# Kernel tuning notes

Measured on AMD Instinct MI355X. Metric: run time of the kernel, lower is better.

## Reference

```python
import jax, jax.numpy as jnp
import numpy as np

EPS = 1e-5

def rmsnorm(x, w):
    var = jnp.mean(x * x, axis=-1, keepdims=True)
    return x * jax.lax.rsqrt(var + EPS) * w

def apply_rope(x, cos, sin):
    # x: [B, S, H, D], cos/sin: [S, D//2]; llama-style complex rotation over pairs
    B, S, H, D = x.shape
    xr = x.reshape(B, S, H, D // 2, 2)
    x0, x1 = xr[..., 0], xr[..., 1]
    c = cos[None, :, None, :]
    s = sin[None, :, None, :]
    o0 = x0 * c - x1 * s
    o1 = x0 * s + x1 * c
    return jnp.stack([o0, o1], axis=-1).reshape(B, S, H, D)

def setup_inputs() -> dict:
    key = jax.random.key(0)
    ks = jax.random.split(key, 8)
    B, S, dim = 2, 2048, 2048
    H, nope, rope = 16, 128, 64
    q_lr, kv_lr = 1536, 512
    hd = nope + rope
    x = jax.random.normal(ks[0], (B, S, dim), jnp.float32)
    wd_q = jax.random.normal(ks[1], (dim, q_lr), jnp.float32) * (dim ** -0.5)
    wu_q = jax.random.normal(ks[2], (q_lr, H * hd), jnp.float32) * (q_lr ** -0.5)
    q_norm_w = jnp.ones((q_lr,), jnp.float32)
    wd_kv = jax.random.normal(ks[3], (dim, kv_lr + rope), jnp.float32) * (dim ** -0.5)
    wu_kv = jax.random.normal(ks[4], (kv_lr, H * 2 * nope), jnp.float32) * (kv_lr ** -0.5)
    kv_norm_w = jnp.ones((kv_lr,), jnp.float32)
    wo = jax.random.normal(ks[5], (H * nope, dim), jnp.float32) * ((H * nope) ** -0.5)
    pos = jnp.arange(S, dtype=jnp.float32)
    inv_freq = 1.0 / (10000.0 ** (jnp.arange(0, rope, 2, dtype=jnp.float32) / rope))
    ang = pos[:, None] * inv_freq[None, :]  # [S, rope//2]
    return {"x": x, "wd_q": wd_q, "wu_q": wu_q, "q_norm_w": q_norm_w,
            "wd_kv": wd_kv, "wu_kv": wu_kv, "kv_norm_w": kv_norm_w, "wo": wo,
            "cos": jnp.cos(ang), "sin": jnp.sin(ang), "start_pos": 0}

def reference(x, wd_q, wu_q, q_norm_w, wd_kv, wu_kv, kv_norm_w, wo, cos, sin, start_pos):
    B, S, dim = x.shape
    H, nope, rope = 16, 128, 64
    kv_lr = 512
    hd = nope + rope
    # low-rank Q projection + RMSNorm
    cq = x @ wd_q
    xq = rmsnorm(cq, q_norm_w) @ wu_q
    xq = xq.reshape(B, S, H, hd)
    xq_nope, xq_rope = xq[..., :nope], xq[..., nope:]
    # low-rank KV projection
    kvd = x @ wd_kv
    ckv, xk_rope = kvd[..., :kv_lr], kvd[..., kv_lr:]
    xk_rope = xk_rope.reshape(B, S, 1, rope)
    kvu = (rmsnorm(ckv, kv_norm_w) @ wu_kv).reshape(B, S, H, 2 * nope)
    xk_nope, xv = kvu[..., :nope], kvu[..., nope:]
    # partial RoPE
    xq_rope = apply_rope(xq_rope, cos, sin)
    xk_rope = apply_rope(xk_rope, cos, sin)
    xk_rope = jnp.broadcast_to(xk_rope, (B, S, H, rope))
    q = jnp.concatenate([xq_nope, xq_rope], axis=-1)  # [B,S,H,192]
    k = jnp.concatenate([xk_nope, xk_rope], axis=-1)
    # causal SDPA
    scale = 1.0 / jnp.sqrt(jnp.float32(hd))
    scores = jnp.einsum('bqhd,bkhd->bhqk', q, k) * scale
    mask = jnp.tril(jnp.ones((S, S), bool))
    scores = jnp.where(mask[None, None], scores, jnp.finfo(scores.dtype).min)
    attn = jax.nn.softmax(scores, axis=-1)
    out = jnp.einsum('bhqk,bkhd->bqhd', attn, xv).reshape(B, S, H * nope)
    return out @ wo
```

## Files before the change

### kernel.cpp

```cpp
#include <hip/hip_runtime.h>
#include <hip/hip_bf16.h>

#define S_LEN 2048
#define NHEAD 16
#define NOPE 128
#define ROPE 64
#define HD 192

typedef unsigned short ushort_t;
typedef __attribute__((ext_vector_type(8))) short short8;
typedef __attribute__((ext_vector_type(4))) float f32x4;

#define AS1 __attribute__((address_space(1)))
#define AS3 __attribute__((address_space(3)))

__device__ __forceinline__ unsigned short f2bf(float f) {
  unsigned int u = __float_as_uint(f);
  return (unsigned short)((u + 0x7FFFu + ((u >> 16) & 1u)) >> 16);
}

__global__ __launch_bounds__(256) void prep_k(const float* __restrict__ x, ushort_t* __restrict__ xb,
                                              const float* __restrict__ wd_q, ushort_t* __restrict__ wdqt,
                                              const float* __restrict__ wd_kv, ushort_t* __restrict__ wdkvt,
                                              const float* __restrict__ wu_q, ushort_t* __restrict__ wuqt,
                                              const float* __restrict__ wu_kv, ushort_t* __restrict__ wukvt,
                                              const float* __restrict__ wo, ushort_t* __restrict__ wot) {
  int id = blockIdx.x;
  if (id < 4096) {
    const int i = id * 256 + threadIdx.x;
    const float4 v0 = *(const float4*)&x[(size_t)i * 8];
    const float4 v1 = *(const float4*)&x[(size_t)i * 8 + 4];
    union { uint4 u; ushort_t s[8]; } pk;
    pk.s[0] = f2bf(v0.x); pk.s[1] = f2bf(v0.y); pk.s[2] = f2bf(v0.z); pk.s[3] = f2bf(v0.w);
    pk.s[4] = f2bf(v1.x); pk.s[5] = f2bf(v1.y); pk.s[6] = f2bf(v1.z); pk.s[7] = f2bf(v1.w);
    *(uint4*)&xb[(size_t)i * 8] = pk.u;
    return;
  }
  id -= 4096;
  const float* B; ushort_t* Bt; int K, N, gx;
  if (id < 3072)               { B = wd_q;  Bt = wdqt;  K = 2048; N = 1536; gx = 48;  }
  else if ((id -= 3072) < 1280){ B = wd_kv; Bt = wdkvt; K = 2048; N = 576;  gx = 20;  }
  else if ((id -= 1280) < 4608){ B = wu_q;  Bt = wuqt;  K = 1536; N = 3072; gx = 96;  }
  else if ((id -= 4608) < 2048){ B = wu_kv; Bt = wukvt; K = 512;  N = 4096; gx = 128; }
  else { id -= 2048;             B = wo;    Bt = wot;   K = 2048; N = 2048; gx = 64;  }
  __shared__ float tile[32][33];
  const int tx = threadIdx.x & 31, ty = threadIdx.x >> 5;
  const int n0 = (id % gx) * 32, k0 = (id / gx) * 32;
  if (n0 >= N) {
#pragma unroll
    for (int r = 0; r < 4; ++r)
      Bt[(size_t)(n0 + ty + 8 * r) * K + k0 + tx] = 0;
    return;
  }
#pragma unroll
  for (int r = 0; r < 4; ++r)
    tile[ty + 8 * r][tx] = B[(size_t)(k0 + ty + 8 * r) * N + n0 + tx];
  __syncthreads();
#pragma unroll
  for (int r = 0; r < 4; ++r)
    Bt[(size_t)(n0 + ty + 8 * r) * K + k0 + tx] = f2bf(tile[tx][ty + 8 * r]);
}

template<int EPI>
__global__ __launch_bounds__(256) void mfma_gemm(const ushort_t* __restrict__ A,
                                                 const ushort_t* __restrict__ Bt,
                                                 float* __restrict__ C,
                                                 int M, int N, int K, int ldc,
                                                 ushort_t* __restrict__ kb16o,
                                                 ushort_t* __restrict__ vto,
                                                 float* __restrict__ C2,
                                                 const float* __restrict__ cosb,
                                                 const float* __restrict__ sinb) {
  __shared__ ushort_t As[128 * 32];
  __shared__ ushort_t Bs[128 * 32];
  const int tid = threadIdx.x;
  const int lane = tid & 63;
  const int wave = tid >> 6;
  const int wm = wave & 1, wn = wave >> 1;

  unsigned bxu = blockIdx.x, byu = blockIdx.y;
  {
    const unsigned gx = gridDim.x;
    const unsigned nwg = gx * gridDim.y;
    if ((nwg & 7u) == 0u) {
      unsigned flat = byu * gx + bxu;
      const unsigned cpx = nwg >> 3;
      flat = (flat & 7u) * cpx + (flat >> 3);
      bxu = flat % gx; byu = flat / gx;
    }
  }
  const int m0 = byu * 128, n0 = bxu * 128;
  const int l15 = lane & 15, quad = lane >> 4;

  f32x4 acc[4][4] = {};

  const int it0 = tid, it1 = tid + 256;
  const int ma0 = it0 >> 2, kc0 = it0 & 3;
  const int ma1 = it1 >> 2, kc1 = it1 & 3;

  typedef AS3 ushort_t lds_us;
  lds_us* AsL = (lds_us*)As;
  lds_us* BsL = (lds_us*)Bs;
  const int wbase = wave * 512;

  for (int k0 = 0; k0 < K; k0 += 32) {
    __builtin_amdgcn_global_load_lds(
        (const AS1 void*)&A[(size_t)(m0 + ma0) * K + k0 + kc0 * 8],
        (AS3 void*)(AsL + wbase), 16, 0, 0);
    __builtin_amdgcn_global_load_lds(
        (const AS1 void*)&A[(size_t)(m0 + ma1) * K + k0 + kc1 * 8],
        (AS3 void*)(AsL + 2048 + wbase), 16, 0, 0);
    __builtin_amdgcn_global_load_lds(
        (const AS1 void*)&Bt[(size_t)(n0 + ma0) * K + k0 + kc0 * 8],
        (AS3 void*)(BsL + wbase), 16, 0, 0);
    __builtin_amdgcn_global_load_lds(
        (const AS1 void*)&Bt[(size_t)(n0 + ma1) * K + k0 + kc1 * 8],
        (AS3 void*)(BsL + 2048 + wbase), 16, 0, 0);
    __syncthreads();

    short8 af[4], bf[4];
#pragma unroll
    for (int i = 0; i < 4; ++i)
      af[i] = *(const short8*)&As[(wm * 64 + i * 16 + l15) * 32 + quad * 8];
#pragma unroll
    for (int j = 0; j < 4; ++j)
      bf[j] = *(const short8*)&Bs[(wn * 64 + j * 16 + l15) * 32 + quad * 8];
#pragma unroll
    for (int i = 0; i < 4; ++i)
#pragma unroll
      for (int j = 0; j < 4; ++j)
        acc[i][j] = __builtin_amdgcn_mfma_f32_16x16x32_bf16(af[i], bf[j], acc[i][j], 0, 0, 0);
    __syncthreads();
  }

  if constexpr (EPI == 0) {
#pragma unroll
    for (int i = 0; i < 4; ++i)
#pragma unroll
      for (int r = 0; r < 4; ++r) {
        const size_t rg = (size_t)(m0 + wm * 64 + i * 16 + quad * 4 + r);
#pragma unroll
        for (int j = 0; j < 4; ++j)
          C[rg * ldc + n0 + wn * 64 + j * 16 + l15] = acc[i][j][r];
      }
  } else if constexpr (EPI == 1) {
    const int h = n0 >> 8;
    const bool is_v = (n0 >> 7) & 1;
    if (!is_v) {
#pragma unroll
      for (int i = 0; i < 4; ++i)
#pragma unroll
        for (int r = 0; r < 4; ++r) {
          const size_t rg = (size_t)(m0 + wm * 64 + i * 16 + quad * 4 + r);
#pragma unroll
          for (int j = 0; j < 4; ++j)
            kb16o[rg * 2048 + h * 128 + wn * 64 + j * 16 + l15] = f2bf(acc[i][j][r]);
        }
    } else {
      __shared__ __align__(16) ushort_t trb[64 * 136];
      const int bb = m0 >> 11;
      const int m0loc = m0 & 2047;
      ushort_t* vbase = vto + ((size_t)(bb * NHEAD + h) * 128) * 2048;
#pragma unroll
      for (int vh = 0; vh < 2; ++vh) {
        if (wn == vh) {
#pragma unroll
          for (int i = 0; i < 4; ++i)
#pragma unroll
            for (int r = 0; r < 4; ++r) {
              const int tloc = wm * 64 + i * 16 + quad * 4 + r;
#pragma unroll
              for (int j = 0; j < 4; ++j)
                trb[(j * 16 + l15) * 136 + tloc] = f2bf(acc[i][j][r]);
            }
        }
        __syncthreads();
#pragma unroll
        for (int it = 0; it < 4; ++it) {
          const int u = tid + (it << 8);
          const int vdl = u >> 4, tc = u & 15;
          *(uint4*)&vbase[(size_t)(vh * 64 + vdl) * 2048 + m0loc + tc * 8] =
              *(const uint4*)&trb[vdl * 136 + tc * 8];
        }
        __syncthreads();
      }
    }
  } else if constexpr (EPI == 2) {
    float* Cd;
    int ldd, nc;
    if (n0 < 1536) { Cd = C;  ldd = 1536; nc = n0; }
    else           { Cd = C2; ldd = 640;  nc = n0 - 1536; }
#pragma unroll
    for (int i = 0; i < 4; ++i)
#pragma unroll
      for (int r = 0; r < 4; ++r) {
        const size_t rg = (size_t)(m0 + wm * 64 + i * 16 + quad * 4 + r);
#pragma unroll
        for (int j = 0; j < 4; ++j)
          Cd[rg * ldd + nc + wn * 64 + j * 16 + l15] = acc[i][j][r];
      }
  } else {
    const float qscale = 0.07216878364870323f;
#pragma unroll
    for (int i = 0; i < 4; ++i)
#pragma unroll
      for (int r = 0; r < 4; ++r) {
        const int rg = m0 + wm * 64 + i * 16 + quad * 4 + r;
        const int sp = rg & (S_LEN - 1);
#pragma unroll
        for (int j = 0; j < 4; ++j) {
          const int col = n0 + wn * 64 + j * 16 + l15;
          float val = acc[i][j][r] * qscale;
          const float pr = __shfl_xor(val, 1);
          const int dd = col % HD;
          float o = val;
          if (dd >= NOPE) {
            const int d = (dd - NOPE) >> 1;
            const float cc = cosb[sp * 32 + d];
            const float sn = sinb[sp * 32 + d];
            o = (lane & 1) ? (pr * sn + val * cc) : (val * cc - pr * sn);
          }
          kb16o[(size_t)rg * 3072 + col] = f2bf(o);
        }
      }
  }
}

__global__ __launch_bounds__(256) void rmsnorm2_k(const float* __restrict__ cq,
                                                  ushort_t* __restrict__ cqn,
                                                  const float* __restrict__ qw,
                                                  const float* __restrict__ kvd,
                                                  ushort_t* __restrict__ ckvn,
                                                  const float* __restrict__ kvw) {
  const bool is_q = blockIdx.x < 4096;
  const int row = blockIdx.x & 4095;
  const int tid = threadIdx.x;
  const float* ip = is_q ? cq + (size_t)row * 1536 : kvd + (size_t)row * 640;
  ushort_t* op = is_q ? cqn + (size_t)row * 1536 : ckvn + (size_t)row * 512;
  const float* w = is_q ? qw : kvw;
  const int L = is_q ? 1536 : 512;
  const int nper = L >> 8;
  float r[6];
  float ss = 0.f;
  for (int j = 0; j < nper; ++j) {
    r[j] = ip[tid + (j << 8)];
    ss += r[j] * r[j];
  }
  for (int off = 32; off; off >>= 1) ss += __shfl_down(ss, off);
  __shared__ float wsum[4];
  __shared__ float scale_s;
  if ((tid & 63) == 0) wsum[tid >> 6] = ss;
  __syncthreads();
  if (tid == 0) {
    float t = wsum[0] + wsum[1] + wsum[2] + wsum[3];
    scale_s = rsqrtf(t / (float)L + 1e-5f);
  }
  __syncthreads();
  const float sc = scale_s;
  for (int j = 0; j < nper; ++j)
    op[tid + (j << 8)] = f2bf(r[j] * sc * w[tid + (j << 8)]);
}

__global__ __launch_bounds__(256) void rope_kr_k(const float* __restrict__ kvd,
                                                 ushort_t* __restrict__ krope16,
                                                 const float* __restrict__ cosb,
                                                 const float* __restrict__ sinb) {
  const int tid = threadIdx.x;
  const int row = blockIdx.x * 8 + (tid >> 5);
  const int d = tid & 31;
  const int s = row & (S_LEN - 1);
  const float c = cosb[s * 32 + d];
  const float sn = sinb[s * 32 + d];
  const float* kb = kvd + (size_t)row * 640 + 512;
  const float y0 = kb[2 * d], y1 = kb[2 * d + 1];
  union { unsigned int u; ushort_t s2[2]; } pk;
  pk.s2[0] = f2bf(y0 * c - y1 * sn);
  pk.s2[1] = f2bf(y0 * sn + y1 * c);
  *(unsigned int*)&krope16[(size_t)row * 64 + 2 * d] = pk.u;
}

#define QT 128
#define KC 64
__global__ __launch_bounds__(256, 2) void attn_k(const ushort_t* __restrict__ q16,
                                                 const ushort_t* __restrict__ kb16,
                                                 const ushort_t* __restrict__ vT,
                                                 const ushort_t* __restrict__ krope16,
                                                 ushort_t* __restrict__ outp) {
  const int bx = blockIdx.x;
  const int g = bx & 31;
  const int s = bx >> 5;
  const int tile = (s < 8) ? s : 23 - s;
  const int b = g >> 4, h = g & 15;
  const int q0 = tile * QT;
  const int tid = threadIdx.x;
  const int lane = tid & 63;
  const int wq = tid >> 6;
  const int l15 = lane & 15, quad = lane >> 4;

  __shared__ __align__(16) ushort_t Kn[64 * 128];
  __shared__ __align__(16) ushort_t Kr[64 * 64];
  __shared__ __align__(16) ushort_t Vt[2][128 * 64];
  __shared__ __align__(16) ushort_t Pb[4][32 * 72];

  const int qbase = q0 + wq * 32;
  const size_t growq = (size_t)b * S_LEN + qbase;
  const ushort_t* vTh = vT + ((size_t)(b * NHEAD + h) * 128) * 2048;
  const size_t bbase = (size_t)b * S_LEN;

  typedef AS3 ushort_t lds_us;
  lds_us* KnL = (lds_us*)Kn;
  lds_us* KrL = (lds_us*)Kr;
  lds_us* VtL = (lds_us*)Vt;
  const int wbase = wq * 512;

  auto issueK = [&](int c) {
    const size_t growk = bbase + (size_t)c * KC;
#pragma unroll
    for (int it = 0; it < 4; ++it) {
      const int u = tid + (it << 8);
      const int key = u >> 4, sl = u & 15;
      const int ss = sl ^ (key & 7);
      __builtin_amdgcn_global_load_lds(
          (const AS1 void*)&kb16[(growk + key) * 2048 + h * 128 + ss * 8],
          (AS3 void*)(KnL + wbase + it * 2048), 16, 0, 0);
    }
#pragma unroll
    for (int it = 0; it < 2; ++it) {
      const int u = tid + (it << 8);
      const int key = u >> 3, sl = u & 7;
      const int ss = sl ^ (key & 7);
      __builtin_amdgcn_global_load_lds(
          (const AS1 void*)&krope16[(growk + key) * 64 + ss * 8],
          (AS3 void*)(KrL + wbase + it * 2048), 16, 0, 0);
    }
  };
  auto issueV = [&](int c, int buf) {
    const int j0 = c * KC;
#pragma unroll
    for (int it = 0; it < 4; ++it) {
      const int u = tid + (it << 8);
      const int vd = u >> 3, sl = u & 7;
      const int ss = sl ^ (vd & 7);
      __builtin_amdgcn_global_load_lds(
          (const AS1 void*)&vTh[(size_t)vd * 2048 + j0 + ss * 8],
          (AS3 void*)(VtL + buf * 8192 + wbase + it * 2048), 16, 0, 0);
    }
  };

  issueK(0);
  issueV(0, 0);
  __builtin_amdgcn_sched_barrier(0);

  short8 qf[2][6];
#pragma unroll
  for (int mt = 0; mt < 2; ++mt)
#pragma unroll
    for (int ks = 0; ks < 6; ++ks)
      qf[mt][ks] = *(const short8*)&q16[(growq + mt * 16 + l15) * 3072 + h * HD + ks * 32 + quad * 8];

  f32x4 oacc[2][8] = {};
  float mrow[2][4], lrow[2][4];
  int q_r[2][4];
#pragma unroll
  for (int mt = 0; mt < 2; ++mt)
#pragma unroll
    for (int r = 0; r < 4; ++r) {
      mrow[mt][r] = -1e30f; lrow[mt][r] = 0.f;
      q_r[mt][r] = qbase + mt * 16 + quad * 4 + r;
    }

  const int nchunk = (q0 + QT) / KC;

  asm volatile("s_waitcnt vmcnt(4)" ::: "memory");
  __builtin_amdgcn_s_barrier();
  __builtin_amdgcn_sched_barrier(0);

  for (int c = 0; c < nchunk; ++c) {
    const int j0 = c * KC;
    const bool more = (c + 1 < nchunk);
    const int buf = c & 1;
    const bool skipw = (j0 > qbase + 31);

    f32x4 sacc[2][4] = {};
    if (!skipw) {
      __builtin_amdgcn_s_setprio(1);
#pragma unroll
      for (int ks = 0; ks < 6; ++ks) {
        short8 kf[4];
        if (ks < 4) {
#pragma unroll
          for (int kt = 0; kt < 4; ++kt)
            kf[kt] = *(const short8*)&Kn[(kt * 16 + l15) * 128 + (((ks * 4 + quad) ^ (l15 & 7)) << 3)];
        } else {
#pragma unroll
          for (int kt = 0; kt < 4; ++kt)
            kf[kt] = *(const short8*)&Kr[(kt * 16 + l15) * 64 + ((((ks - 4) * 4 + quad) ^ (l15 & 7)) << 3)];
        }
#pragma unroll
        for (int mt = 0; mt < 2; ++mt)
#pragma unroll
          for (int kt = 0; kt < 4; ++kt)
            sacc[mt][kt] = __builtin_amdgcn_mfma_f32_16x16x32_bf16(qf[mt][ks], kf[kt], sacc[mt][kt], 0, 0, 0);
      }
      __builtin_amdgcn_s_setprio(0);
    }

    __builtin_amdgcn_s_barrier();
    if (more) issueK(c + 1);
    __builtin_amdgcn_sched_barrier(0);

    if (!skipw) {
      if (j0 + KC - 1 > qbase) {
#pragma unroll
        for (int mt = 0; mt < 2; ++mt)
#pragma unroll
          for (int kt = 0; kt < 4; ++kt) {
            const int key = j0 + kt * 16 + l15;
#pragma unroll
            for (int r = 0; r < 4; ++r)
              sacc[mt][kt][r] = (key <= q_r[mt][r]) ? sacc[mt][kt][r] : -1e30f;
          }
      }
      float pmax[2][4];
#pragma unroll
      for (int mt = 0; mt < 2; ++mt)
#pragma unroll
        for (int r = 0; r < 4; ++r) {
          float mx = fmaxf(fmaxf(sacc[mt][0][r], sacc[mt][1][r]),
                           fmaxf(sacc[mt][2][r], sacc[mt][3][r]));
          mx = fmaxf(mx, __shfl_xor(mx, 1));
          mx = fmaxf(mx, __shfl_xor(mx, 2));
          mx = fmaxf(mx, __shfl_xor(mx, 4));
          mx = fmaxf(mx, __shfl_xor(mx, 8));
          pmax[mt][r] = mx;
        }
      bool need = false;
#pragma unroll
      for (int mt = 0; mt < 2; ++mt)
#pragma unroll
        for (int r = 0; r < 4; ++r)
          need = need || (pmax[mt][r] > mrow[mt][r] + 8.0f);
      const bool upd = __any(need);
      float alpha[2][4];
      if (upd) {
#pragma unroll
        for (int mt = 0; mt < 2; ++mt)
#pragma unroll
          for (int r = 0; r < 4; ++r) {
            const float mn = fmaxf(mrow[mt][r], pmax[mt][r]);
            alpha[mt][r] = __expf(mrow[mt][r] - mn);
            mrow[mt][r] = mn;
          }
      }
#pragma unroll
      for (int mt = 0; mt < 2; ++mt)
#pragma unroll
        for (int kt = 0; kt < 4; ++kt)
#pragma unroll
          for (int r = 0; r < 4; ++r)
            sacc[mt][kt][r] = __expf(sacc[mt][kt][r] - mrow[mt][r]);
#pragma unroll
      for (int mt = 0; mt < 2; ++mt)
#pragma unroll
        for (int r = 0; r < 4; ++r) {
          float rs = sacc[mt][0][r] + sacc[mt][1][r] + sacc[mt][2][r] + sacc[mt][3][r];
          rs += __shfl_xor(rs, 1);
          rs += __shfl_xor(rs, 2);
          rs += __shfl_xor(rs, 4);
          rs += __shfl_xor(rs, 8);
          lrow[mt][r] = upd ? lrow[mt][r] * alpha[mt][r] + rs : lrow[mt][r] + rs;
        }
#pragma unroll
      for (int mt = 0; mt < 2; ++mt)
#pragma unroll
        for (int kt = 0; kt < 4; ++kt)
#pragma unroll
          for (int r = 0; r < 4; ++r)
            Pb[wq][(mt * 16 + quad * 4 + r) * 72 + kt * 16 + l15] = f2bf(sacc[mt][kt][r]);
      if (upd) {
#pragma unroll
        for (int mt = 0; mt < 2; ++mt)
#pragma unroll
          for (int nt = 0; nt < 8; ++nt)
#pragma unroll
            for (int r = 0; r < 4; ++r)
              oacc[mt][nt][r] *= alpha[mt][r];
      }
    }

    if (more) asm volatile("s_waitcnt vmcnt(6)" ::: "memory");
    else      asm volatile("s_waitcnt vmcnt(0)" ::: "memory");
    __builtin_amdgcn_s_barrier();
    __builtin_amdgcn_sched_barrier(0);

    if (!skipw) {
      __builtin_amdgcn_s_setprio(1);
#pragma unroll
      for (int st = 0; st < 2; ++st) {
        short8 pf[2];
#pragma unroll
        for (int mt = 0; mt < 2; ++mt)
          pf[mt] = *(const short8*)&Pb[wq][(mt * 16 + l15) * 72 + st * 32 + quad * 8];
#pragma unroll
        for (int nt = 0; nt < 8; ++nt) {
          const short8 vf = *(const short8*)&Vt[buf][(nt * 16 + l15) * 64 + (((st * 4 + quad) ^ (l15 & 7)) << 3)];
#pragma unroll
          for (int mt = 0; mt < 2; ++mt)
            oacc[mt][nt] = __builtin_amdgcn_mfma_f32_16x16x32_bf16(pf[mt], vf, oacc[mt][nt], 0, 0, 0);
        }
      }
      __builtin_amdgcn_s_setprio(0);
    }

    if (more) {
      issueV(c + 1, buf ^ 1);
      __builtin_amdgcn_sched_barrier(0);
      asm volatile("s_waitcnt vmcnt(4)" ::: "memory");
      __builtin_amdgcn_s_barrier();
      __builtin_amdgcn_sched_barrier(0);
    }
  }

#pragma unroll
  for (int mt = 0; mt < 2; ++mt)
#pragma unroll
    for (int r = 0; r < 4; ++r) {
      const float inv = 1.0f / lrow[mt][r];
      const size_t orow = growq + mt * 16 + quad * 4 + r;
#pragma unroll
      for (int nt = 0; nt < 8; ++nt)
        outp[orow * 2048 + h * 128 + nt * 16 + l15] = f2bf(oacc[mt][nt][r] * inv);
    }
}

extern "C" void kernel_launch(void* const* d_in, const int* in_sizes, int n_in,
                              void* d_out, int out_size, void* d_ws, size_t ws_size,
                              hipStream_t stream) {
  const float* x        = (const float*)d_in[0];
  const float* wd_q     = (const float*)d_in[1];
  const float* wu_q     = (const float*)d_in[2];
  const float* q_norm_w = (const float*)d_in[3];
  const float* wd_kv    = (const float*)d_in[4];
  const float* wu_kv    = (const float*)d_in[5];
  const float* kv_norm_w= (const float*)d_in[6];
  const float* wo       = (const float*)d_in[7];
  const float* cosb     = (const float*)d_in[8];
  const float* sinb     = (const float*)d_in[9];
  float* out = (float*)d_out;

  char* ws = (char*)d_ws;
  float*    cq    = (float*)(ws + 0);
  ushort_t* q16   = (ushort_t*)(ws + 0);
  ushort_t* kb16  = (ushort_t*)(ws + 50331648);
  ushort_t* vT    = (ushort_t*)(ws + 67108864);
  ushort_t* xb    = (ushort_t*)(ws + 83886080);
  ushort_t* cqn   = (ushort_t*)(ws + 117440512);
  float*    kvd   = (float*)(ws + 130023424);
  ushort_t* ckvn  = (ushort_t*)(ws + 140509184);
  ushort_t* aoutb = (ushort_t*)(ws + 130023424);
  ushort_t* krope16 = (ushort_t*)(ws + 146800640);
  ushort_t* wdqt  = (ushort_t*)(ws + 147849216);
  ushort_t* wdkvt = (ushort_t*)(ws + 154140672);
  ushort_t* wuqt  = (ushort_t*)(ws + 156762112);
  ushort_t* wukvt = (ushort_t*)(ws + 166199296);
  ushort_t* wot   = (ushort_t*)(ws + 170393600);

  const int M = 2 * S_LEN;
  dim3 blk(256);

  prep_k<<<19200, blk, 0, stream>>>(x, xb, wd_q, wdqt, wd_kv, wdkvt,
                                    wu_q, wuqt, wu_kv, wukvt, wo, wot);

  mfma_gemm<2><<<dim3(2176 / 128, M / 128), blk, 0, stream>>>(
      xb, wdqt, cq, M, 2176, 2048, 1536, nullptr, nullptr, kvd, nullptr, nullptr);
  rmsnorm2_k<<<2 * M, 256, 0, stream>>>(cq, cqn, q_norm_w, kvd, ckvn, kv_norm_w);
  mfma_gemm<3><<<dim3(3072 / 128, M / 128), blk, 0, stream>>>(
      cqn, wuqt, nullptr, M, 3072, 1536, 0, q16, nullptr, nullptr, cosb, sinb);
  mfma_gemm<1><<<dim3(4096 / 128, M / 128), blk, 0, stream>>>(
      ckvn, wukvt, nullptr, M, 4096, 512, 0, kb16, vT, nullptr, nullptr, nullptr);
  rope_kr_k<<<512, blk, 0, stream>>>(kvd, krope16, cosb, sinb);
  attn_k<<<2 * NHEAD * (S_LEN / QT), 256, 0, stream>>>(q16, kb16, vT, krope16, aoutb);
  mfma_gemm<0><<<dim3(2048 / 128, M / 128), blk, 0, stream>>>(
      aoutb, wot, out, M, 2048, 2048, 2048, nullptr, nullptr, nullptr, nullptr, nullptr);
}
```

Baseline: 496.5 us.

## Use 8 waves of 16 query rows in attention and fold k-rope into rmsnorm

The attention kernel moves from 4 waves each owning 32 query rows to 8 waves each owning 16 rows in 512-thread blocks. The cooperative K/V loads, wait counts and P staging buffer are resized to match. This roughly halves per-wave register use so more waves can hide latency, and gives finer causal skipping per wave, at the cost of each K/V fragment read from LDS being reused by only one query tile. Separately, the standalone k-rope kernel is folded into the rmsnorm kernel's KV rows to save one launch.

```diff
diff --git a/kernel.cpp b/kernel.cpp
--- a/kernel.cpp
+++ b/kernel.cpp
@@ -231,7 +231,10 @@
                                                   const float* __restrict__ qw,
                                                   const float* __restrict__ kvd,
                                                   ushort_t* __restrict__ ckvn,
-                                                  const float* __restrict__ kvw) {
+                                                  const float* __restrict__ kvw,
+                                                  ushort_t* __restrict__ krope16,
+                                                  const float* __restrict__ cosb,
+                                                  const float* __restrict__ sinb) {
   const bool is_q = blockIdx.x < 4096;
   const int row = blockIdx.x & 4095;
   const int tid = threadIdx.x;
@@ -259,29 +262,23 @@
   const float sc = scale_s;
   for (int j = 0; j < nper; ++j)
     op[tid + (j << 8)] = f2bf(r[j] * sc * w[tid + (j << 8)]);
-}
-
-__global__ __launch_bounds__(256) void rope_kr_k(const float* __restrict__ kvd,
-                                                 ushort_t* __restrict__ krope16,
-                                                 const float* __restrict__ cosb,
-                                                 const float* __restrict__ sinb) {
-  const int tid = threadIdx.x;
-  const int row = blockIdx.x * 8 + (tid >> 5);
-  const int d = tid & 31;
-  const int s = row & (S_LEN - 1);
-  const float c = cosb[s * 32 + d];
-  const float sn = sinb[s * 32 + d];
-  const float* kb = kvd + (size_t)row * 640 + 512;
-  const float y0 = kb[2 * d], y1 = kb[2 * d + 1];
-  union { unsigned int u; ushort_t s2[2]; } pk;
-  pk.s2[0] = f2bf(y0 * c - y1 * sn);
-  pk.s2[1] = f2bf(y0 * sn + y1 * c);
-  *(unsigned int*)&krope16[(size_t)row * 64 + 2 * d] = pk.u;
+  if (!is_q && tid < 32) {
+    const int d = tid;
+    const int s = row & (S_LEN - 1);
+    const float c = cosb[s * 32 + d];
+    const float sn = sinb[s * 32 + d];
+    const float* kb = kvd + (size_t)row * 640 + 512;
+    const float y0 = kb[2 * d], y1 = kb[2 * d + 1];
+    union { unsigned int u; ushort_t s2[2]; } pk;
+    pk.s2[0] = f2bf(y0 * c - y1 * sn);
+    pk.s2[1] = f2bf(y0 * sn + y1 * c);
+    *(unsigned int*)&krope16[(size_t)row * 64 + 2 * d] = pk.u;
+  }
 }
 
 #define QT 128
 #define KC 64
-__global__ __launch_bounds__(256, 2) void attn_k(const ushort_t* __restrict__ q16,
+__global__ __launch_bounds__(512, 4) void attn_k(const ushort_t* __restrict__ q16,
                                                  const ushort_t* __restrict__ kb16,
                                                  const ushort_t* __restrict__ vT,
                                                  const ushort_t* __restrict__ krope16,
@@ -300,9 +297,9 @@
   __shared__ __align__(16) ushort_t Kn[64 * 128];
   __shared__ __align__(16) ushort_t Kr[64 * 64];
   __shared__ __align__(16) ushort_t Vt[2][128 * 64];
-  __shared__ __align__(16) ushort_t Pb[4][32 * 72];
-
-  const int qbase = q0 + wq * 32;
+  __shared__ __align__(16) ushort_t Pb[8][16 * 72];
+
+  const int qbase = q0 + wq * 16;
   const size_t growq = (size_t)b * S_LEN + qbase;
   const ushort_t* vTh = vT + ((size_t)(b * NHEAD + h) * 128) * 2048;
   const size_t bbase = (size_t)b * S_LEN;
@@ -316,34 +313,33 @@
   auto issueK = [&](int c) {
     const size_t growk = bbase + (size_t)c * KC;
 #pragma unroll
-    for (int it = 0; it < 4; ++it) {
-      const int u = tid + (it << 8);
+    for (int it = 0; it < 2; ++it) {
+      const int u = tid + (it << 9);
       const int key = u >> 4, sl = u & 15;
       const int ss = sl ^ (key & 7);
       __builtin_amdgcn_global_load_lds(
           (const AS1 void*)&kb16[(growk + key) * 2048 + h * 128 + ss * 8],
-          (AS3 void*)(KnL + wbase + it * 2048), 16, 0, 0);
-    }
-#pragma unroll
-    for (int it = 0; it < 2; ++it) {
-      const int u = tid + (it << 8);
+          (AS3 void*)(KnL + wbase + it * 4096), 16, 0, 0);
+    }
+    {
+      const int u = tid;
       const int key = u >> 3, sl = u & 7;
       const int ss = sl ^ (key & 7);
       __builtin_amdgcn_global_load_lds(
           (const AS1 void*)&krope16[(growk + key) * 64 + ss * 8],
-          (AS3 void*)(KrL + wbase + it * 2048), 16, 0, 0);
+          (AS3 void*)(KrL + wbase), 16, 0, 0);
     }
   };
   auto issueV = [&](int c, int buf) {
     const int j0 = c * KC;
 #pragma unroll
-    for (int it = 0; it < 4; ++it) {
-      const int u = tid + (it << 8);
+    for (int it = 0; it < 2; ++it) {
+      const int u = tid + (it << 9);
       const int vd = u >> 3, sl = u & 7;
       const int ss = sl ^ (vd & 7);
       __builtin_amdgcn_global_load_lds(
           (const AS1 void*)&vTh[(size_t)vd * 2048 + j0 + ss * 8],
-          (AS3 void*)(VtL + buf * 8192 + wbase + it * 2048), 16, 0, 0);
+          (AS3 void*)(VtL + buf * 8192 + wbase + it * 4096), 16, 0, 0);
     }
   };
 
@@ -351,27 +347,23 @@
   issueV(0, 0);
   __builtin_amdgcn_sched_barrier(0);
 
-  short8 qf[2][6];
-#pragma unroll
-  for (int mt = 0; mt < 2; ++mt)
-#pragma unroll
-    for (int ks = 0; ks < 6; ++ks)
-      qf[mt][ks] = *(const short8*)&q16[(growq + mt * 16 + l15) * 3072 + h * HD + ks * 32 + quad * 8];
-
-  f32x4 oacc[2][8] = {};
-  float mrow[2][4], lrow[2][4];
-  int q_r[2][4];
-#pragma unroll
-  for (int mt = 0; mt < 2; ++mt)
-#pragma unroll
-    for (int r = 0; r < 4; ++r) {
-      mrow[mt][r] = -1e30f; lrow[mt][r] = 0.f;
-      q_r[mt][r] = qbase + mt * 16 + quad * 4 + r;
-    }
+  short8 qf[6];
+#pragma unroll
+  for (int ks = 0; ks < 6; ++ks)
+    qf[ks] = *(const short8*)&q16[(growq + l15) * 3072 + h * HD + ks * 32 + quad * 8];
+
+  f32x4 oacc[8] = {};
+  float mrow[4], lrow[4];
+  int q_r[4];
+#pragma unroll
+  for (int r = 0; r < 4; ++r) {
+    mrow[r] = -1e30f; lrow[r] = 0.f;
+    q_r[r] = qbase + quad * 4 + r;
+  }
 
   const int nchunk = (q0 + QT) / KC;
 
-  asm volatile("s_waitcnt vmcnt(4)" ::: "memory");
+  asm volatile("s_waitcnt vmcnt(2)" ::: "memory");
   __builtin_amdgcn_s_barrier();
   __builtin_amdgcn_sched_barrier(0);
 
@@ -379,9 +371,9 @@
     const int j0 = c * KC;
     const bool more = (c + 1 < nchunk);
     const int buf = c & 1;
-    const bool skipw = (j0 > qbase + 31);
-
-    f32x4 sacc[2][4] = {};
+    const bool skipw = (j0 > qbase + 15);
+
+    f32x4 sacc[4] = {};
     if (!skipw) {
       __builtin_amdgcn_s_setprio(1);
 #pragma unroll
@@ -397,10 +389,8 @@
             kf[kt] = *(const short8*)&Kr[(kt * 16 + l15) * 64 + ((((ks - 4) * 4 + quad) ^ (l15 & 7)) << 3)];
         }
 #pragma unroll
-        for (int mt = 0; mt < 2; ++mt)
-#pragma unroll
-          for (int kt = 0; kt < 4; ++kt)
-            sacc[mt][kt] = __builtin_amdgcn_mfma_f32_16x16x32_bf16(qf[mt][ks], kf[kt], sacc[mt][kt], 0, 0, 0);
+        for (int kt = 0; kt < 4; ++kt)
+          sacc[kt] = __builtin_amdgcn_mfma_f32_16x16x32_bf16(qf[ks], kf[kt], sacc[kt], 0, 0, 0);
       }
       __builtin_amdgcn_s_setprio(0);
     }
@@ -412,83 +402,67 @@
     if (!skipw) {
       if (j0 + KC - 1 > qbase) {
 #pragma unroll
-        for (int mt = 0; mt < 2; ++mt)
-#pragma unroll
-          for (int kt = 0; kt < 4; ++kt) {
-            const int key = j0 + kt * 16 + l15;
-#pragma unroll
-            for (int r = 0; r < 4; ++r)
-              sacc[mt][kt][r] = (key <= q_r[mt][r]) ? sacc[mt][kt][r] : -1e30f;
-          }
-      }
-      float pmax[2][4];
-#pragma unroll
-      for (int mt = 0; mt < 2; ++mt)
+        for (int kt = 0; kt < 4; ++kt) {
+          const int key = j0 + kt * 16 + l15;
+#pragma unroll
+          for (int r = 0; r < 4; ++r)
+            sacc[kt][r] = (key <= q_r[r]) ? sacc[kt][r] : -1e30f;
+        }
+      }
+      float pmax[4];
+#pragma unroll
+      for (int r = 0; r < 4; ++r) {
+        float mx = fmaxf(fmaxf(sacc[0][r], sacc[1][r]),
+                         fmaxf(sacc[2][r], sacc[3][r]));
+        mx = fmaxf(mx, __shfl_xor(mx, 1));
+        mx = fmaxf(mx, __shfl_xor(mx, 2));
+        mx = fmaxf(mx, __shfl_xor(mx, 4));
+        mx = fmaxf(mx, __shfl_xor(mx, 8));
+        pmax[r] = mx;
+      }
+      bool need = false;
+#pragma unroll
+      for (int r = 0; r < 4; ++r)
+        need = need || (pmax[r] > mrow[r] + 8.0f);
+      const bool upd = __any(need);
+      float alpha[4];
+      if (upd) {
 #pragma unroll
         for (int r = 0; r < 4; ++r) {
-          float mx = fmaxf(fmaxf(sacc[mt][0][r], sacc[mt][1][r]),
-                           fmaxf(sacc[mt][2][r], sacc[mt][3][r]));
-          mx = fmaxf(mx, __shfl_xor(mx, 1));
-          mx = fmaxf(mx, __shfl_xor(mx, 2));
-          mx = fmaxf(mx, __shfl_xor(mx, 4));
-          mx = fmaxf(mx, __shfl_xor(mx, 8));
-          pmax[mt][r] = mx;
-        }
-      bool need = false;
-#pragma unroll
-      for (int mt = 0; mt < 2; ++mt)
+          const float mn = fmaxf(mrow[r], pmax[r]);
+          alpha[r] = __expf(mrow[r] - mn);
+          mrow[r] = mn;
+        }
+      }
+#pragma unroll
+      for (int kt = 0; kt < 4; ++kt)
 #pragma unroll
         for (int r = 0; r < 4; ++r)
-          need = need || (pmax[mt][r] > mrow[mt][r] + 8.0f);
-      const bool upd = __any(need);
-      float alpha[2][4];
+          sacc[kt][r] = __expf(sacc[kt][r] - mrow[r]);
+#pragma unroll
+      for (int r = 0; r < 4; ++r) {
+        float rs = sacc[0][r] + sacc[1][r] + sacc[2][r] + sacc[3][r];
+        rs += __shfl_xor(rs, 1);
+        rs += __shfl_xor(rs, 2);
+        rs += __shfl_xor(rs, 4);
+        rs += __shfl_xor(rs, 8);
+        lrow[r] = upd ? lrow[r] * alpha[r] + rs : lrow[r] + rs;
+      }
+#pragma unroll
+      for (int kt = 0; kt < 4; ++kt)
+#pragma unroll
+        for (int r = 0; r < 4; ++r)
+          Pb[wq][(quad * 4 + r) * 72 + kt * 16 + l15] = f2bf(sacc[kt][r]);
       if (upd) {
 #pragma unroll
-        for (int mt = 0; mt < 2; ++mt)
-#pragma unroll
-          for (int r = 0; r < 4; ++r) {
-            const float mn = fmaxf(mrow[mt][r], pmax[mt][r]);
-            alpha[mt][r] = __expf(mrow[mt][r] - mn);
-            mrow[mt][r] = mn;
-          }
-      }
-#pragma unroll
-      for (int mt = 0; mt < 2; ++mt)
-#pragma unroll
-        for (int kt = 0; kt < 4; ++kt)
+        for (int nt = 0; nt < 8; ++nt)
 #pragma unroll
           for (int r = 0; r < 4; ++r)
-            sacc[mt][kt][r] = __expf(sacc[mt][kt][r] - mrow[mt][r]);
-#pragma unroll
-      for (int mt = 0; mt < 2; ++mt)
-#pragma unroll
-        for (int r = 0; r < 4; ++r) {
-          float rs = sacc[mt][0][r] + sacc[mt][1][r] + sacc[mt][2][r] + sacc[mt][3][r];
-          rs += __shfl_xor(rs, 1);
-          rs += __shfl_xor(rs, 2);
-          rs += __shfl_xor(rs, 4);
-          rs += __shfl_xor(rs, 8);
-          lrow[mt][r] = upd ? lrow[mt][r] * alpha[mt][r] + rs : lrow[mt][r] + rs;
-        }
-#pragma unroll
-      for (int mt = 0; mt < 2; ++mt)
-#pragma unroll
-        for (int kt = 0; kt < 4; ++kt)
-#pragma unroll
-          for (int r = 0; r < 4; ++r)
-            Pb[wq][(mt * 16 + quad * 4 + r) * 72 + kt * 16 + l15] = f2bf(sacc[mt][kt][r]);
-      if (upd) {
-#pragma unroll
-        for (int mt = 0; mt < 2; ++mt)
-#pragma unroll
-          for (int nt = 0; nt < 8; ++nt)
-#pragma unroll
-            for (int r = 0; r < 4; ++r)
-              oacc[mt][nt][r] *= alpha[mt][r];
-      }
-    }
-
-    if (more) asm volatile("s_waitcnt vmcnt(6)" ::: "memory");
+            oacc[nt][r] *= alpha[r];
+      }
+    }
+
+    if (more) asm volatile("s_waitcnt vmcnt(3)" ::: "memory");
     else      asm volatile("s_waitcnt vmcnt(0)" ::: "memory");
     __builtin_amdgcn_s_barrier();
     __builtin_amdgcn_sched_barrier(0);
@@ -497,16 +471,11 @@
       __builtin_amdgcn_s_setprio(1);
 #pragma unroll
       for (int st = 0; st < 2; ++st) {
-        short8 pf[2];
-#pragma unroll
-        for (int mt = 0; mt < 2; ++mt)
-          pf[mt] = *(const short8*)&Pb[wq][(mt * 16 + l15) * 72 + st * 32 + quad * 8];
+        const short8 pf = *(const short8*)&Pb[wq][l15 * 72 + st * 32 + quad * 8];
 #pragma unroll
         for (int nt = 0; nt < 8; ++nt) {
           const short8 vf = *(const short8*)&Vt[buf][(nt * 16 + l15) * 64 + (((st * 4 + quad) ^ (l15 & 7)) << 3)];
-#pragma unroll
-          for (int mt = 0; mt < 2; ++mt)
-            oacc[mt][nt] = __builtin_amdgcn_mfma_f32_16x16x32_bf16(pf[mt], vf, oacc[mt][nt], 0, 0, 0);
+          oacc[nt] = __builtin_amdgcn_mfma_f32_16x16x32_bf16(pf, vf, oacc[nt], 0, 0, 0);
         }
       }
       __builtin_amdgcn_s_setprio(0);
@@ -515,22 +484,20 @@
     if (more) {
       issueV(c + 1, buf ^ 1);
       __builtin_amdgcn_sched_barrier(0);
-      asm volatile("s_waitcnt vmcnt(4)" ::: "memory");
+      asm volatile("s_waitcnt vmcnt(2)" ::: "memory");
       __builtin_amdgcn_s_barrier();
       __builtin_amdgcn_sched_barrier(0);
     }
   }
 
 #pragma unroll
-  for (int mt = 0; mt < 2; ++mt)
-#pragma unroll
-    for (int r = 0; r < 4; ++r) {
-      const float inv = 1.0f / lrow[mt][r];
-      const size_t orow = growq + mt * 16 + quad * 4 + r;
-#pragma unroll
-      for (int nt = 0; nt < 8; ++nt)
-        outp[orow * 2048 + h * 128 + nt * 16 + l15] = f2bf(oacc[mt][nt][r] * inv);
-    }
+  for (int r = 0; r < 4; ++r) {
+    const float inv = 1.0f / lrow[r];
+    const size_t orow = growq + quad * 4 + r;
+#pragma unroll
+    for (int nt = 0; nt < 8; ++nt)
+      outp[orow * 2048 + h * 128 + nt * 16 + l15] = f2bf(oacc[nt][r] * inv);
+  }
 }
 
 extern "C" void kernel_launch(void* const* d_in, const int* in_sizes, int n_in,
@@ -573,13 +540,13 @@
 
   mfma_gemm<2><<<dim3(2176 / 128, M / 128), blk, 0, stream>>>(
       xb, wdqt, cq, M, 2176, 2048, 1536, nullptr, nullptr, kvd, nullptr, nullptr);
-  rmsnorm2_k<<<2 * M, 256, 0, stream>>>(cq, cqn, q_norm_w, kvd, ckvn, kv_norm_w);
+  rmsnorm2_k<<<2 * M, 256, 0, stream>>>(cq, cqn, q_norm_w, kvd, ckvn, kv_norm_w,
+                                        krope16, cosb, sinb);
   mfma_gemm<3><<<dim3(3072 / 128, M / 128), blk, 0, stream>>>(
       cqn, wuqt, nullptr, M, 3072, 1536, 0, q16, nullptr, nullptr, cosb, sinb);
   mfma_gemm<1><<<dim3(4096 / 128, M / 128), blk, 0, stream>>>(
       ckvn, wukvt, nullptr, M, 4096, 512, 0, kb16, vT, nullptr, nullptr, nullptr);
-  rope_kr_k<<<512, blk, 0, stream>>>(kvd, krope16, cosb, sinb);
-  attn_k<<<2 * NHEAD * (S_LEN / QT), 256, 0, stream>>>(q16, kb16, vT, krope16, aoutb);
+  attn_k<<<2 * NHEAD * (S_LEN / QT), 512, 0, stream>>>(q16, kb16, vT, krope16, aoutb);
   mfma_gemm<0><<<dim3(2048 / 128, M / 128), blk, 0, stream>>>(
       aoutb, wot, out, M, 2048, 2048, 2048, nullptr, nullptr, nullptr, nullptr, nullptr);
 }
```

Measured after the change: 482.6 us. 2.8% less time.
